# Performance work log

Hardware: AMD Instinct MI355X
Metric: run time of the kernel (lower is better)

The kernel has to match this reference:

```python
import jax, jax.numpy as jnp
import numpy as np

D_MODEL = 1024
D_STATE = 16
D_CONV = 4
EXPAND = 2
N_LAYERS = 4
D_INNER = EXPAND * D_MODEL          # 2048
DT_RANK = (D_MODEL + 15) // 16     # 64
BATCH, SEQ = 2, 1024
LN_EPS = 1e-5


def setup_inputs() -> dict:
    key = jax.random.key(0)
    ks = jax.random.split(key, 10)
    s = 0.02
    A_log = jnp.log(jnp.broadcast_to(
        jnp.arange(1, D_STATE + 1, dtype=jnp.float32), (N_LAYERS, D_INNER, D_STATE)))
    return {
        "x": jax.random.normal(ks[0], (BATCH, SEQ, D_MODEL), jnp.float32),
        "in_proj_w": jax.random.normal(ks[1], (N_LAYERS, 2 * D_INNER, D_MODEL), jnp.float32) * s,
        "conv_w": jax.random.normal(ks[2], (N_LAYERS, D_INNER, D_CONV), jnp.float32) * s,
        "conv_b": jnp.zeros((N_LAYERS, D_INNER), jnp.float32),
        "x_proj_w": jax.random.normal(ks[3], (N_LAYERS, DT_RANK + 2 * D_STATE, D_INNER), jnp.float32) * s,
        "dt_proj_w": jax.random.normal(ks[4], (N_LAYERS, D_INNER, DT_RANK), jnp.float32) * s,
        "dt_proj_b": jax.random.uniform(ks[5], (N_LAYERS, D_INNER), jnp.float32, -5.0, -3.0),
        "A_log": A_log,
        "D_skip": jnp.ones((N_LAYERS, D_INNER), jnp.float32),
        "out_proj_w": jax.random.normal(ks[6], (N_LAYERS, D_MODEL, D_INNER), jnp.float32) * s,
        "ln_g": jnp.ones((D_MODEL,), jnp.float32),
        "ln_b": jnp.zeros((D_MODEL,), jnp.float32),
    }


def _layer_norm(x, g, b):
    mu = jnp.mean(x, axis=-1, keepdims=True)
    var = jnp.mean(jnp.square(x - mu), axis=-1, keepdims=True)
    return (x - mu) * jax.lax.rsqrt(var + LN_EPS) * g + b


def _scan_combine(e1, e2):
    a1, b1 = e1
    a2, b2 = e2
    return a1 * a2, a2 * b1 + b2


def _mamba_block(x, in_w, cw, cb, xp_w, dt_w, dt_b, A_log, D_skip, out_w):
    # x: [B, L, D]
    xz = jnp.einsum('bld,ed->ble', x, in_w)          # [B, L, 2*d_inner]
    xm, z = jnp.split(xz, 2, axis=-1)
    # causal depthwise conv over time
    xc = jnp.transpose(xm, (0, 2, 1))                 # [B, d_inner, L]
    xc = jax.lax.conv_general_dilated(
        xc, cw[:, None, :], window_strides=(1,), padding=[(D_CONV - 1, 0)],
        feature_group_count=D_INNER, dimension_numbers=('NCH', 'OIH', 'NCH'))
    xm = jax.nn.silu(jnp.transpose(xc, (0, 2, 1)) + cb[None, None, :])
    # input-dependent dt, B, C
    xdbl = jnp.einsum('bld,ed->ble', xm, xp_w)        # [B, L, dt_rank + 2*S]
    dt, Bm, Cm = jnp.split(xdbl, [DT_RANK, DT_RANK + D_STATE], axis=-1)
    dt = jax.nn.softplus(jnp.einsum('blr,dr->bld', dt, dt_w) + dt_b)   # [B, L, d_inner]
    A = -jnp.exp(A_log)                               # [d_inner, S]
    dA = jnp.exp(dt[..., None] * A)                   # [B, L, d_inner, S]
    dBu = dt[..., None] * Bm[:, :, None, :] * xm[..., None]
    # selective scan: h_t = dA_t * h_{t-1} + dBu_t, via associative scan over L
    _, h = jax.lax.associative_scan(_scan_combine, (dA, dBu), axis=1)
    y = jnp.einsum('blds,bls->bld', h, Cm) + xm * D_skip
    y = y * jax.nn.silu(z)
    return jnp.einsum('bld,od->blo', y, out_w)        # [B, L, D]


def reference(x, in_proj_w, conv_w, conv_b, x_proj_w, dt_proj_w, dt_proj_b,
              A_log, D_skip, out_proj_w, ln_g, ln_b):
    for i in range(N_LAYERS):
        x = x + _mamba_block(_layer_norm(x, ln_g, ln_b),
                             in_proj_w[i], conv_w[i], conv_b[i], x_proj_w[i],
                             dt_proj_w[i], dt_proj_b[i], A_log[i], D_skip[i],
                             out_proj_w[i])
    return _layer_norm(x, ln_g, ln_b)
```

## Files before the change

kernel.cpp:

```cpp
#include <hip/hip_runtime.h>

#define NTOK 2048
#define SEQL 1024
#define DMODEL 1024
#define DINNER 2048
#define DSTATE 16
#define DTRANK 64
#define GCH 64
#define LC 16
#define XDS 128
#define XSPK 8

typedef __attribute__((ext_vector_type(8))) short short8;
typedef __attribute__((ext_vector_type(4))) float float4v;

__device__ __forceinline__ unsigned short f2bf(float f) {
    unsigned u = __float_as_uint(f);
    unsigned r = u + 0x7FFFu + ((u >> 16) & 1u);
    return (unsigned short)(r >> 16);
}
__device__ __forceinline__ float bf2f(unsigned short h) {
    return __uint_as_float(((unsigned)h) << 16);
}

__global__ __launch_bounds__(256) void f32_to_bf16_4(
    const float* __restrict__ s0, unsigned short* __restrict__ d0, int c0,
    const float* __restrict__ s1, unsigned short* __restrict__ d1, int c1,
    const float* __restrict__ s2, unsigned short* __restrict__ d2, int c2,
    const float* __restrict__ s3, unsigned short* __restrict__ d3, int c3) {
    int i = blockIdx.x * 256 + threadIdx.x;
    if (i >= c3) return;
    const float* s; unsigned short* dd; int j;
    if (i < c0)      { s = s0; dd = d0; j = i; }
    else if (i < c1) { s = s1; dd = d1; j = i - c0; }
    else if (i < c2) { s = s2; dd = d2; j = i - c1; }
    else             { s = s3; dd = d3; j = i - c2; }
    float4 a = ((const float4*)s)[2 * j];
    float4 b = ((const float4*)s)[2 * j + 1];
    uint4 v;
    v.x = (unsigned)f2bf(a.x) | ((unsigned)f2bf(a.y) << 16);
    v.y = (unsigned)f2bf(a.z) | ((unsigned)f2bf(a.w) << 16);
    v.z = (unsigned)f2bf(b.x) | ((unsigned)f2bf(b.y) << 16);
    v.w = (unsigned)f2bf(b.z) | ((unsigned)f2bf(b.w) << 16);
    ((uint4*)dd)[j] = v;
}

__global__ __launch_bounds__(256) void ln_kernel(
    const float* __restrict__ x, float* __restrict__ x_copy,
    const float* __restrict__ g, const float* __restrict__ b,
    unsigned short* __restrict__ out_bf) {
    int row = blockIdx.x;
    int t = threadIdx.x;
    float4 v = ((const float4*)(x + (size_t)row * DMODEL))[t];
    ((float4*)(x_copy + (size_t)row * DMODEL))[t] = v;
    float s  = v.x + v.y + v.z + v.w;
    float ss = v.x*v.x + v.y*v.y + v.z*v.z + v.w*v.w;
    for (int o = 32; o; o >>= 1) { s += __shfl_xor(s, o); ss += __shfl_xor(ss, o); }
    __shared__ float red[8];
    int wv = t >> 6;
    if ((t & 63) == 0) { red[wv * 2] = s; red[wv * 2 + 1] = ss; }
    __syncthreads();
    s  = red[0] + red[2] + red[4] + red[6];
    ss = red[1] + red[3] + red[5] + red[7];
    float mu = s * (1.f / DMODEL);
    float rstd = rsqrtf(ss * (1.f / DMODEL) - mu * mu + 1e-5f);
    float4 gv = ((const float4*)g)[t];
    float4 bv = ((const float4*)b)[t];
    ((ushort4*)out_bf)[row * 256 + t] = make_ushort4(
        f2bf((v.x - mu) * rstd * gv.x + bv.x),
        f2bf((v.y - mu) * rstd * gv.y + bv.y),
        f2bf((v.z - mu) * rstd * gv.z + bv.z),
        f2bf((v.w - mu) * rstd * gv.w + bv.w));
}

__global__ __launch_bounds__(256) void residual_ln(
    float* __restrict__ x_res, const float* __restrict__ p0,
    const float* __restrict__ p1, const float* __restrict__ p2,
    const float* __restrict__ p3, const float* __restrict__ g,
    const float* __restrict__ b, unsigned short* __restrict__ out_bf,
    float* __restrict__ out_f32) {
    int row = blockIdx.x;
    int t = threadIdx.x;
    size_t o4 = (size_t)row * 256 + t;
    float4 v  = ((const float4*)x_res)[o4];
    float4 a0 = ((const float4*)p0)[o4];
    float4 a1 = ((const float4*)p1)[o4];
    float4 a2 = ((const float4*)p2)[o4];
    float4 a3 = ((const float4*)p3)[o4];
    v.x += (a0.x + a1.x) + (a2.x + a3.x);
    v.y += (a0.y + a1.y) + (a2.y + a3.y);
    v.z += (a0.z + a1.z) + (a2.z + a3.z);
    v.w += (a0.w + a1.w) + (a2.w + a3.w);
    ((float4*)x_res)[o4] = v;
    float s  = v.x + v.y + v.z + v.w;
    float ss = v.x*v.x + v.y*v.y + v.z*v.z + v.w*v.w;
    for (int o = 32; o; o >>= 1) { s += __shfl_xor(s, o); ss += __shfl_xor(ss, o); }
    __shared__ float red[8];
    int wv = t >> 6;
    if ((t & 63) == 0) { red[wv * 2] = s; red[wv * 2 + 1] = ss; }
    __syncthreads();
    s  = red[0] + red[2] + red[4] + red[6];
    ss = red[1] + red[3] + red[5] + red[7];
    float mu = s * (1.f / DMODEL);
    float rstd = rsqrtf(ss * (1.f / DMODEL) - mu * mu + 1e-5f);
    float4 gv = ((const float4*)g)[t];
    float4 bv = ((const float4*)b)[t];
    float o0 = (v.x - mu) * rstd * gv.x + bv.x;
    float o1 = (v.y - mu) * rstd * gv.y + bv.y;
    float o2 = (v.z - mu) * rstd * gv.z + bv.z;
    float o3 = (v.w - mu) * rstd * gv.w + bv.w;
    if (out_f32) {
        ((float4*)out_f32)[o4] = make_float4(o0, o1, o2, o3);
    } else {
        ((ushort4*)out_bf)[o4] = make_ushort4(f2bf(o0), f2bf(o1), f2bf(o2), f2bf(o3));
    }
}

#define BKG 32
__global__ __launch_bounds__(256) void gemm64(
    const unsigned short* __restrict__ A, const unsigned short* __restrict__ B,
    void* __restrict__ Cv, const float* __restrict__ bias,
    int M, int N, int K, int Nb, int mode) {
    __shared__ __attribute__((aligned(16))) unsigned short As[3][128 * BKG];
    __shared__ __attribute__((aligned(16))) unsigned short Bs[3][64 * BKG];
    int m0 = blockIdx.y * 128, n0 = blockIdx.x * 64;
    int Klocal = K / gridDim.z;
    int kstart = blockIdx.z * Klocal;
    int t = threadIdx.x;
    int lane = t & 63, w = t >> 6;
    int tr = lane & 15, quad = lane >> 4;
    int r_l = lane >> 2;
    int q_l = (lane & 3) ^ ((lane >> 3) & 3);
    int col_l = q_l * 8;

    float4v acc[2][4];
    for (int mi = 0; mi < 2; ++mi)
        for (int ni = 0; ni < 4; ++ni)
            acc[mi][ni] = (float4v){0.f, 0.f, 0.f, 0.f};

    auto stage = [&](int kt, int buf) {
        int kbase = kstart + kt * BKG;
#pragma unroll
        for (int j = 0; j < 2; ++j) {
            int c = w * 2 + j;
            const unsigned short* ga = A + (size_t)(m0 + c * 16 + r_l) * K + kbase + col_l;
            __builtin_amdgcn_global_load_lds(
                (const __attribute__((address_space(1))) void*)ga,
                (__attribute__((address_space(3))) void*)(&As[buf][c * 512]),
                16, 0, 0);
        }
        int brow = n0 + w * 16 + r_l;
        if (brow >= Nb) brow = Nb - 1;
        const unsigned short* gb = B + (size_t)brow * K + kbase + col_l;
        __builtin_amdgcn_global_load_lds(
            (const __attribute__((address_space(1))) void*)gb,
            (__attribute__((address_space(3))) void*)(&Bs[buf][w * 512]),
            16, 0, 0);
    };

    int KT = Klocal / BKG;
    stage(0, 0);
    if (KT > 1) stage(1, 1);
    int u_off = (tr * 4 + (quad ^ ((tr >> 1) & 3))) * 8;
    for (int kt = 0; kt < KT; ++kt) {
        int cur = kt % 3;
        if (kt + 2 < KT) stage(kt + 2, (kt + 2) % 3);
        asm volatile("" ::: "memory");
        int nleft = KT - kt - 1;
        if (nleft >= 2)      __builtin_amdgcn_s_waitcnt(0x0F76);
        else if (nleft == 1) __builtin_amdgcn_s_waitcnt(0x0F73);
        else                 __builtin_amdgcn_s_waitcnt(0x0F70);
        __builtin_amdgcn_s_barrier();
        asm volatile("" ::: "memory");
        short8 af[2], bfr[4];
#pragma unroll
        for (int i = 0; i < 2; ++i)
            af[i] = *(const short8*)(&As[cur][(w * 2 + i) * 512 + u_off]);
#pragma unroll
        for (int i = 0; i < 4; ++i)
            bfr[i] = *(const short8*)(&Bs[cur][i * 512 + u_off]);
#pragma unroll
        for (int mi = 0; mi < 2; ++mi)
#pragma unroll
            for (int ni = 0; ni < 4; ++ni)
                acc[mi][ni] = __builtin_amdgcn_mfma_f32_16x16x32_bf16(
                    af[mi], bfr[ni], acc[mi][ni], 0, 0, 0);
        asm volatile("" ::: "memory");
        __builtin_amdgcn_s_barrier();
        asm volatile("" ::: "memory");
    }
    size_t zoff = (size_t)blockIdx.z * M * N;
    for (int mi = 0; mi < 2; ++mi)
        for (int ni = 0; ni < 4; ++ni) {
            int col = n0 + ni * 16 + tr;
            int rowb = m0 + w * 32 + mi * 16 + quad * 4;
            for (int r = 0; r < 4; ++r) {
                size_t off = (size_t)(rowb + r) * N + col;
                float val = acc[mi][ni][r];
                if (mode == 0) {
                    ((float*)Cv)[zoff + off] = val;
                } else if (mode == 2) {
                    ((unsigned short*)Cv)[off] = f2bf(val);
                } else {
                    float v2 = val + bias[col];
                    float sp = (v2 > 15.f) ? v2 : log1pf(expf(v2));
                    ((unsigned short*)Cv)[off] = f2bf(sp);
                }
            }
        }
}

__global__ __launch_bounds__(256) void reduce_xp(
    const float* __restrict__ part, unsigned short* __restrict__ dtA,
    float* __restrict__ BC) {
    int i = blockIdx.x * 256 + threadIdx.x;
    int row = i >> 7, col = i & 127;
    float s = 0.f;
#pragma unroll
    for (int z = 0; z < XSPK; ++z)
        s += part[(size_t)z * NTOK * XDS + i];
    if (col < 64) dtA[row * 64 + col] = f2bf(s);
    else if (col < 96) BC[row * 32 + (col - 64)] = s;
}

__global__ __launch_bounds__(256) void conv_silu(
    const unsigned short* __restrict__ xz, const float* __restrict__ cw,
    const float* __restrict__ cb, unsigned short* __restrict__ xm_bf) {
    int i = blockIdx.x * 256 + threadIdx.x;
    int c8 = i & (DINNER / 8 - 1);
    int tk = i >> 8;
    int l = tk & (SEQL - 1);
    int c = c8 * 8;
    const unsigned short* base = xz + (size_t)tk * (2 * DINNER) + c;
    short8 r3 = {0,0,0,0,0,0,0,0}, r2 = {0,0,0,0,0,0,0,0}, r1 = {0,0,0,0,0,0,0,0};
    if (l >= 3) r3 = *(const short8*)(base - 3 * 2 * DINNER);
    if (l >= 2) r2 = *(const short8*)(base - 2 * 2 * DINNER);
    if (l >= 1) r1 = *(const short8*)(base - 1 * 2 * DINNER);
    short8 r0 = *(const short8*)(base);
    short8 out;
#pragma unroll
    for (int j = 0; j < 8; ++j) {
        float4 wv = ((const float4*)cw)[c + j];
        float acc = cb[c + j]
            + bf2f((unsigned short)r3[j]) * wv.x
            + bf2f((unsigned short)r2[j]) * wv.y
            + bf2f((unsigned short)r1[j]) * wv.z
            + bf2f((unsigned short)r0[j]) * wv.w;
        float sv = acc / (1.f + expf(-acc));
        out[j] = (short)f2bf(sv);
    }
    *(short8*)(xm_bf + (size_t)tk * DINNER + c) = out;
}

__global__ __launch_bounds__(256) void scan_a(
    const unsigned short* __restrict__ dt_bf, const unsigned short* __restrict__ xm_bf,
    const float* __restrict__ BC, const float* __restrict__ A_log,
    float* __restrict__ h_end, float* __restrict__ S_chunk) {
    int bid = blockIdx.x;
    int g = bid >> 4, b = (bid >> 3) & 1, cbk = bid & 7;
    int c = cbk * 256 + threadIdx.x;
    __shared__ float Bsh[LC][16];
    {
        int li = threadIdx.x >> 4, s = threadIdx.x & 15;
        Bsh[li][s] = BC[((size_t)(b * SEQL + g * LC + li)) * 32 + s];
    }
    __syncthreads();
    float a_l2[16], h[16];
#pragma unroll
    for (int s = 0; s < 16; ++s) {
        a_l2[s] = -expf(A_log[c * 16 + s]) * 1.44269504f;
        h[s] = 0.f;
    }
    float S = 0.f;
    int rowbase = b * SEQL + g * LC;
    for (int i = 0; i < LC; ++i) {
        size_t off = (size_t)(rowbase + i) * DINNER + c;
        float dtv = bf2f(dt_bf[off]);
        S += dtv;
        float u = bf2f(xm_bf[off]);
        float bu = dtv * u;
#pragma unroll
        for (int s = 0; s < 16; ++s) {
            float dA = exp2f(dtv * a_l2[s]);
            h[s] = dA * h[s] + Bsh[i][s] * bu;
        }
    }
    int gb = g * 2 + b;
#pragma unroll
    for (int s = 0; s < 16; ++s)
        h_end[((size_t)gb * 16 + s) * DINNER + c] = h[s];
    S_chunk[(size_t)gb * DINNER + c] = S;
}

__global__ __launch_bounds__(256) void scan_b(
    const float* __restrict__ A_log, const float* __restrict__ S_chunk,
    const float* __restrict__ h_end, float* __restrict__ h_in) {
    int idx = blockIdx.x * 256 + threadIdx.x;
    int c = idx & (DINNER - 1);
    int s = (idx >> 11) & 15;
    int b = idx >> 15;
    float a_l2 = -expf(A_log[c * 16 + s]) * 1.44269504f;
    float h = 0.f;
    for (int g = 0; g < GCH; ++g) {
        int gb = g * 2 + b;
        h_in[((size_t)gb * 16 + s) * DINNER + c] = h;
        float P = exp2f(a_l2 * S_chunk[(size_t)gb * DINNER + c]);
        h = P * h + h_end[((size_t)gb * 16 + s) * DINNER + c];
    }
}

__global__ __launch_bounds__(256) void scan_c(
    const unsigned short* __restrict__ dt_bf, const unsigned short* __restrict__ xm_bf,
    const float* __restrict__ BC, const float* __restrict__ A_log,
    const float* __restrict__ D_skip, const unsigned short* __restrict__ xz,
    const float* __restrict__ h_in, unsigned short* __restrict__ y_bf) {
    int bid = blockIdx.x;
    int g = bid >> 4, b = (bid >> 3) & 1, cbk = bid & 7;
    int c = cbk * 256 + threadIdx.x;
    __shared__ float BCsh[LC][32];
    for (int r = 0; r < 2; ++r) {
        int e = threadIdx.x + r * 256;
        int li = e >> 5, s = e & 31;
        BCsh[li][s] = BC[((size_t)(b * SEQL + g * LC + li)) * 32 + s];
    }
    __syncthreads();
    int gb = g * 2 + b;
    float a_l2[16], h[16];
#pragma unroll
    for (int s = 0; s < 16; ++s) {
        a_l2[s] = -expf(A_log[c * 16 + s]) * 1.44269504f;
        h[s] = h_in[((size_t)gb * 16 + s) * DINNER + c];
    }
    float dsk = D_skip[c];
    int rowbase = b * SEQL + g * LC;
    for (int i = 0; i < LC; ++i) {
        size_t off = (size_t)(rowbase + i) * DINNER + c;
        float dtv = bf2f(dt_bf[off]);
        float u = bf2f(xm_bf[off]);
        float bu = dtv * u;
        float y = 0.f;
#pragma unroll
        for (int s = 0; s < 16; ++s) {
            float dA = exp2f(dtv * a_l2[s]);
            h[s] = dA * h[s] + BCsh[i][s] * bu;
            y += h[s] * BCsh[i][16 + s];
        }
        y += u * dsk;
        float zv = bf2f(xz[(size_t)(rowbase + i) * (2 * DINNER) + DINNER + c]);
        y *= zv / (1.f + expf(-zv));
        y_bf[off] = f2bf(y);
    }
}

extern "C" void kernel_launch(void* const* d_in, const int* in_sizes, int n_in,
                              void* d_out, int out_size, void* d_ws, size_t ws_size,
                              hipStream_t stream) {
    const float* x_in   = (const float*)d_in[0];
    const float* in_w   = (const float*)d_in[1];
    const float* conv_w = (const float*)d_in[2];
    const float* conv_b = (const float*)d_in[3];
    const float* xp_w   = (const float*)d_in[4];
    const float* dt_w   = (const float*)d_in[5];
    const float* dt_b   = (const float*)d_in[6];
    const float* A_logp = (const float*)d_in[7];
    const float* Dsk    = (const float*)d_in[8];
    const float* out_w  = (const float*)d_in[9];
    const float* ln_g   = (const float*)d_in[10];
    const float* ln_b   = (const float*)d_in[11];
    float* outp = (float*)d_out;

    char* p = (char*)d_ws;
    auto alloc = [&](size_t bytes) {
        void* r = (void*)p;
        p += (bytes + 255) & ~(size_t)255;
        return r;
    };
    float* x_res  = (float*)alloc((size_t)NTOK * DMODEL * 4);
    unsigned short* xn_bf = (unsigned short*)alloc((size_t)NTOK * DMODEL * 2);
    unsigned short* xz_bf = (unsigned short*)alloc((size_t)NTOK * 2 * DINNER * 2);
    unsigned short* xm_bf = (unsigned short*)alloc((size_t)NTOK * DINNER * 2);
    float* xp_part = (float*)alloc((size_t)XSPK * NTOK * XDS * 4);
    float* out_part = (float*)alloc((size_t)4 * NTOK * DMODEL * 4);
    float* BC     = (float*)alloc((size_t)NTOK * 32 * 4);
    unsigned short* dtA_bf = (unsigned short*)alloc((size_t)NTOK * DTRANK * 2);
    unsigned short* dt_bf = (unsigned short*)alloc((size_t)NTOK * DINNER * 2);
    unsigned short* y_bf = (unsigned short*)alloc((size_t)NTOK * DINNER * 2);
    float* h_end  = (float*)alloc((size_t)GCH * 2 * 16 * DINNER * 4);
    float* h_in   = (float*)alloc((size_t)GCH * 2 * 16 * DINNER * 4);
    float* S_chunk = (float*)alloc((size_t)GCH * 2 * DINNER * 4);
    int n_inw  = 4 * 2 * DINNER * DMODEL;
    int n_xpw  = 4 * 96 * DINNER;
    int n_dtw  = 4 * DINNER * DTRANK;
    int n_outw = 4 * DMODEL * DINNER;
    unsigned short* wbf_in  = (unsigned short*)alloc((size_t)n_inw * 2);
    unsigned short* wbf_xp  = (unsigned short*)alloc((size_t)n_xpw * 2);
    unsigned short* wbf_dt  = (unsigned short*)alloc((size_t)n_dtw * 2);
    unsigned short* wbf_out = (unsigned short*)alloc((size_t)n_outw * 2);

    int c0 = n_inw / 8;
    int c1 = c0 + n_xpw / 8;
    int c2 = c1 + n_dtw / 8;
    int c3 = c2 + n_outw / 8;
    f32_to_bf16_4<<<(c3 + 255) / 256, 256, 0, stream>>>(
        in_w, wbf_in, c0, xp_w, wbf_xp, c1, dt_w, wbf_dt, c2, out_w, wbf_out, c3);

    ln_kernel<<<NTOK, 256, 0, stream>>>(x_in, x_res, ln_g, ln_b, xn_bf);

    for (int L = 0; L < 4; ++L) {
        const unsigned short* w_in  = wbf_in  + (size_t)L * 2 * DINNER * DMODEL;
        const float*          w_cv  = conv_w  + (size_t)L * DINNER * 4;
        const float*          b_cv  = conv_b  + (size_t)L * DINNER;
        const unsigned short* w_xp  = wbf_xp  + (size_t)L * 96 * DINNER;
        const unsigned short* w_dt  = wbf_dt  + (size_t)L * DINNER * DTRANK;
        const float*          b_dt  = dt_b    + (size_t)L * DINNER;
        const float*          al    = A_logp  + (size_t)L * DINNER * DSTATE;
        const float*          dskl  = Dsk     + (size_t)L * DINNER;
        const unsigned short* w_out = wbf_out + (size_t)L * DMODEL * DINNER;

        gemm64<<<dim3(64, 16, 1), 256, 0, stream>>>(
            xn_bf, w_in, xz_bf, nullptr, NTOK, 2 * DINNER, DMODEL, 2 * DINNER, 2);
        conv_silu<<<NTOK * (DINNER / 8) / 256, 256, 0, stream>>>(xz_bf, w_cv, b_cv, xm_bf);
        gemm64<<<dim3(2, 16, XSPK), 256, 0, stream>>>(
            xm_bf, w_xp, xp_part, nullptr, NTOK, XDS, DINNER, 96, 0);
        reduce_xp<<<NTOK * XDS / 256, 256, 0, stream>>>(xp_part, dtA_bf, BC);
        gemm64<<<dim3(32, 16, 1), 256, 0, stream>>>(
            dtA_bf, w_dt, dt_bf, b_dt, NTOK, DINNER, DTRANK, DINNER, 3);
        scan_a<<<GCH * 16, 256, 0, stream>>>(dt_bf, xm_bf, BC, al, h_end, S_chunk);
        scan_b<<<2 * 16 * DINNER / 256, 256, 0, stream>>>(al, S_chunk, h_end, h_in);
        scan_c<<<GCH * 16, 256, 0, stream>>>(dt_bf, xm_bf, BC, al, dskl, xz_bf,
                                             h_in, y_bf);
        gemm64<<<dim3(16, 16, 4), 256, 0, stream>>>(
            y_bf, w_out, out_part, nullptr, NTOK, DMODEL, DINNER, DMODEL, 0);
        residual_ln<<<NTOK, 256, 0, stream>>>(
            x_res, out_part, out_part + (size_t)NTOK * DMODEL,
            out_part + (size_t)2 * NTOK * DMODEL, out_part + (size_t)3 * NTOK * DMODEL,
            ln_g, ln_b, (L < 3) ? xn_bf : nullptr, (L < 3) ? nullptr : outp);
    }
}
```

Before: 873.5 us.

## Accumulate out_proj split-K partials atomically into residual; widen weight conversion

The out_proj GEMM no longer writes four split-K fp32 partial buffers that a separate kernel sums into the residual. It now atomically adds each partial into x_res, so the LayerNorm kernel only reads the residual. This removes the partial-buffer write and four-way read traffic. In exchange it adds fp32 atomic contention and makes the summation order nondeterministic. The weight fp32-to-bf16 conversion kernel also handles 16 elements per thread instead of 8.

```diff
diff --git a/kernel.cpp b/kernel.cpp
--- a/kernel.cpp
+++ b/kernel.cpp
@@ -35,14 +35,21 @@
     else if (i < c1) { s = s1; dd = d1; j = i - c0; }
     else if (i < c2) { s = s2; dd = d2; j = i - c1; }
     else             { s = s3; dd = d3; j = i - c2; }
-    float4 a = ((const float4*)s)[2 * j];
-    float4 b = ((const float4*)s)[2 * j + 1];
-    uint4 v;
-    v.x = (unsigned)f2bf(a.x) | ((unsigned)f2bf(a.y) << 16);
-    v.y = (unsigned)f2bf(a.z) | ((unsigned)f2bf(a.w) << 16);
-    v.z = (unsigned)f2bf(b.x) | ((unsigned)f2bf(b.y) << 16);
-    v.w = (unsigned)f2bf(b.z) | ((unsigned)f2bf(b.w) << 16);
-    ((uint4*)dd)[j] = v;
+    float4 a = ((const float4*)s)[4 * j];
+    float4 b = ((const float4*)s)[4 * j + 1];
+    float4 c = ((const float4*)s)[4 * j + 2];
+    float4 d = ((const float4*)s)[4 * j + 3];
+    uint4 v0, v1;
+    v0.x = (unsigned)f2bf(a.x) | ((unsigned)f2bf(a.y) << 16);
+    v0.y = (unsigned)f2bf(a.z) | ((unsigned)f2bf(a.w) << 16);
+    v0.z = (unsigned)f2bf(b.x) | ((unsigned)f2bf(b.y) << 16);
+    v0.w = (unsigned)f2bf(b.z) | ((unsigned)f2bf(b.w) << 16);
+    v1.x = (unsigned)f2bf(c.x) | ((unsigned)f2bf(c.y) << 16);
+    v1.y = (unsigned)f2bf(c.z) | ((unsigned)f2bf(c.w) << 16);
+    v1.z = (unsigned)f2bf(d.x) | ((unsigned)f2bf(d.y) << 16);
+    v1.w = (unsigned)f2bf(d.z) | ((unsigned)f2bf(d.w) << 16);
+    ((uint4*)dd)[2 * j]     = v0;
+    ((uint4*)dd)[2 * j + 1] = v1;
 }
 
 __global__ __launch_bounds__(256) void ln_kernel(
@@ -73,25 +80,14 @@
         f2bf((v.w - mu) * rstd * gv.w + bv.w));
 }
 
-__global__ __launch_bounds__(256) void residual_ln(
-    float* __restrict__ x_res, const float* __restrict__ p0,
-    const float* __restrict__ p1, const float* __restrict__ p2,
-    const float* __restrict__ p3, const float* __restrict__ g,
+__global__ __launch_bounds__(256) void ln_only(
+    const float* __restrict__ x_res, const float* __restrict__ g,
     const float* __restrict__ b, unsigned short* __restrict__ out_bf,
     float* __restrict__ out_f32) {
     int row = blockIdx.x;
     int t = threadIdx.x;
     size_t o4 = (size_t)row * 256 + t;
-    float4 v  = ((const float4*)x_res)[o4];
-    float4 a0 = ((const float4*)p0)[o4];
-    float4 a1 = ((const float4*)p1)[o4];
-    float4 a2 = ((const float4*)p2)[o4];
-    float4 a3 = ((const float4*)p3)[o4];
-    v.x += (a0.x + a1.x) + (a2.x + a3.x);
-    v.y += (a0.y + a1.y) + (a2.y + a3.y);
-    v.z += (a0.z + a1.z) + (a2.z + a3.z);
-    v.w += (a0.w + a1.w) + (a2.w + a3.w);
-    ((float4*)x_res)[o4] = v;
+    float4 v = ((const float4*)x_res)[o4];
     float s  = v.x + v.y + v.z + v.w;
     float ss = v.x*v.x + v.y*v.y + v.z*v.z + v.w*v.w;
     for (int o = 32; o; o >>= 1) { s += __shfl_xor(s, o); ss += __shfl_xor(ss, o); }
@@ -201,6 +197,8 @@
                     ((float*)Cv)[zoff + off] = val;
                 } else if (mode == 2) {
                     ((unsigned short*)Cv)[off] = f2bf(val);
+                } else if (mode == 4) {
+                    unsafeAtomicAdd(((float*)Cv) + off, val);
                 } else {
                     float v2 = val + bias[col];
                     float sp = (v2 > 15.f) ? v2 : log1pf(expf(v2));
@@ -380,7 +378,6 @@
     unsigned short* xz_bf = (unsigned short*)alloc((size_t)NTOK * 2 * DINNER * 2);
     unsigned short* xm_bf = (unsigned short*)alloc((size_t)NTOK * DINNER * 2);
     float* xp_part = (float*)alloc((size_t)XSPK * NTOK * XDS * 4);
-    float* out_part = (float*)alloc((size_t)4 * NTOK * DMODEL * 4);
     float* BC     = (float*)alloc((size_t)NTOK * 32 * 4);
     unsigned short* dtA_bf = (unsigned short*)alloc((size_t)NTOK * DTRANK * 2);
     unsigned short* dt_bf = (unsigned short*)alloc((size_t)NTOK * DINNER * 2);
@@ -397,10 +394,10 @@
     unsigned short* wbf_dt  = (unsigned short*)alloc((size_t)n_dtw * 2);
     unsigned short* wbf_out = (unsigned short*)alloc((size_t)n_outw * 2);
 
-    int c0 = n_inw / 8;
-    int c1 = c0 + n_xpw / 8;
-    int c2 = c1 + n_dtw / 8;
-    int c3 = c2 + n_outw / 8;
+    int c0 = n_inw / 16;
+    int c1 = c0 + n_xpw / 16;
+    int c2 = c1 + n_dtw / 16;
+    int c3 = c2 + n_outw / 16;
     f32_to_bf16_4<<<(c3 + 255) / 256, 256, 0, stream>>>(
         in_w, wbf_in, c0, xp_w, wbf_xp, c1, dt_w, wbf_dt, c2, out_w, wbf_out, c3);
 
@@ -430,10 +427,8 @@
         scan_c<<<GCH * 16, 256, 0, stream>>>(dt_bf, xm_bf, BC, al, dskl, xz_bf,
                                              h_in, y_bf);
         gemm64<<<dim3(16, 16, 4), 256, 0, stream>>>(
-            y_bf, w_out, out_part, nullptr, NTOK, DMODEL, DINNER, DMODEL, 0);
-        residual_ln<<<NTOK, 256, 0, stream>>>(
-            x_res, out_part, out_part + (size_t)NTOK * DMODEL,
-            out_part + (size_t)2 * NTOK * DMODEL, out_part + (size_t)3 * NTOK * DMODEL,
-            ln_g, ln_b, (L < 3) ? xn_bf : nullptr, (L < 3) ? nullptr : outp);
-    }
-}
+            y_bf, w_out, x_res, nullptr, NTOK, DMODEL, DINNER, DMODEL, 4);
+        ln_only<<<NTOK, 256, 0, stream>>>(
+            x_res, ln_g, ln_b, (L < 3) ? xn_bf : nullptr, (L < 3) ? nullptr : outp);
+    }
+}
```

After: 928.2 us. 1.06x slower.
